# Kernel optimization log

Measured on AMD Instinct MI355X. Metric: run time of the kernel, lower is better.

The kernel has to match this reference:

```python
import jax, jax.numpy as jnp
import numpy as np

B, S, D = 16, 512, 768      # batch, max_n_words, context_dim (input_size)
E, R = 128, 2048            # entities per doc, candidate relations per doc
H = 768                     # config.hidden_size
H2 = H // 2                 # 384
OUT = 2                     # binary relation classes


def _linear_params(k, fan_in, fan_out):
    k1, k2 = jax.random.split(k)
    bound = 1.0 / np.sqrt(fan_in)
    W = jax.random.uniform(k1, (fan_in, fan_out), minval=-bound, maxval=bound, dtype=jnp.float32)
    b = jax.random.uniform(k2, (fan_out,), minval=-bound, maxval=bound, dtype=jnp.float32)
    return W, b


def setup_inputs() -> dict:
    key = jax.random.key(0)
    ks = jax.random.split(key, 16)
    hW1, hb1 = _linear_params(ks[0], 2 * D, H)
    hW2, hb2 = _linear_params(ks[1], H, H2)
    tW1, tb1 = _linear_params(ks[2], 2 * D, H)
    tW2, tb2 = _linear_params(ks[3], H, H2)
    bnd = 1.0 / np.sqrt(H2)
    bil_w = jax.random.uniform(ks[4], (OUT, H2, H2), minval=-bnd, maxval=bnd, dtype=jnp.float32)
    lW, lb = _linear_params(ks[5], 2 * H2, OUT)
    emb = jax.random.normal(ks[6], (3, D), dtype=jnp.float32)  # entity_emb
    hidden_states = jax.random.normal(ks[7], (B, S, D), dtype=jnp.float32)
    ent_start = jax.random.randint(ks[8], (B, E), 0, S)
    ent_label = jax.random.randint(ks[9], (B, E), 0, 3)
    rel_head = jax.random.randint(ks[10], (B, R), 0, E)
    rel_tail = jax.random.randint(ks[11], (B, R), 0, E)
    rel_label = jax.random.randint(ks[12], (B, R), 0, 2)
    return dict(hidden_states=hidden_states, emb=emb,
                hW1=hW1, hb1=hb1, hW2=hW2, hb2=hb2,
                tW1=tW1, tb1=tb1, tW2=tW2, tb2=tb2,
                bil_w=bil_w, lW=lW, lb=lb,
                ent_start=ent_start, ent_label=ent_label,
                rel_head=rel_head, rel_tail=rel_tail, rel_label=rel_label)


def reference(hidden_states, emb, hW1, hb1, hW2, hb2, tW1, tb1, tW2, tb2,
              bil_w, lW, lb, ent_start, ent_label, rel_head, rel_tail, rel_label):
    def tower(rel_idx, W1, b1, W2, b2):
        start = jnp.take_along_axis(ent_start, rel_idx, axis=1)              # [B,R]
        lab = jnp.take_along_axis(ent_label, rel_idx, axis=1)                # [B,R]
        hid = jnp.take_along_axis(hidden_states, start[..., None], axis=1)   # [B,R,D]
        rep = jnp.concatenate([hid, emb[lab]], axis=-1)                      # [B,R,2D]
        h = jax.nn.relu(rep @ W1 + b1)                                       # [B,R,H]
        return jax.nn.relu(h @ W2 + b2)                                      # [B,R,H2]

    heads = tower(rel_head, hW1, hb1, hW2, hb2)
    tails = tower(rel_tail, tW1, tb1, tW2, tb2)
    # Biaffine: bilinear (no bias) + linear over concat
    logits = (jnp.einsum('bri,oij,brj->bro', heads, bil_w, tails)
              + jnp.concatenate([heads, tails], axis=-1) @ lW + lb)          # [B,R,2]
    logp = jax.nn.log_softmax(logits, axis=-1)
    loss = -jnp.mean(jnp.take_along_axis(logp, rel_label[..., None], axis=-1))
    return loss, logits
```

## Files before the change

### kernel.cpp

```cpp
#include <hip/hip_runtime.h>
#include <hip/hip_bf16.h>
#include <cstdint>

typedef unsigned short ushort_t;
typedef __bf16 bf16x8 __attribute__((ext_vector_type(8)));
typedef float f32x4 __attribute__((ext_vector_type(4)));

#define B_   16
#define S_   512
#define D_   768
#define E_   128
#define R_   2048
#define NREL 32768

__device__ inline ushort_t f2b(float f) {
    uint32_t u = __builtin_bit_cast(uint32_t, f);
    uint32_t r = (u + 0x7fffu + ((u >> 16) & 1u)) >> 16;
    return (ushort_t)r;
}
__device__ inline float b2f(ushort_t u) {
    uint32_t v = ((uint32_t)u) << 16;
    return __builtin_bit_cast(float, v);
}
__device__ inline float bl(uint32_t u) {
    uint32_t v = u << 16;
    return __builtin_bit_cast(float, v);
}
__device__ inline float bh(uint32_t u) {
    uint32_t v = u & 0xffff0000u;
    return __builtin_bit_cast(float, v);
}

__global__ __launch_bounds__(256) void prep_kernel(
    const float* __restrict__ hidden, const float* __restrict__ emb,
    const float* __restrict__ lW,
    const int* __restrict__ ent_start, const int* __restrict__ ent_label,
    ushort_t* __restrict__ repE, ushort_t* __restrict__ BmatT,
    ushort_t* __restrict__ lWtT, float* __restrict__ out)
{
    int idx = blockIdx.x * 256 + threadIdx.x;
    if (idx == 0) out[0] = 0.0f;
    if (idx < 786432) {
        int row = idx / 384, q = idx - row * 384;
        int c = q * 4;
        int b = row >> 7;
        int st = ent_start[row], lab = ent_label[row];
        const float* srcp = (c < 768)
            ? hidden + ((size_t)(b * S_ + st) * D_ + c)
            : emb + ((size_t)lab * D_ + (c - 768));
        float4 v = *reinterpret_cast<const float4*>(srcp);
        uint32_t lo = (uint32_t)f2b(v.x) | ((uint32_t)f2b(v.y) << 16);
        uint32_t hi = (uint32_t)f2b(v.z) | ((uint32_t)f2b(v.w) << 16);
        uint2 pk; pk.x = lo; pk.y = hi;
        *reinterpret_cast<uint2*>(repE + (size_t)idx * 4) = pk;
        return;
    }
    int i2 = idx - 786432;
    if (i2 < 768) {
        int o = i2 / 384, kk = i2 - o * 384;
        BmatT[(768 + o) * 384 + kk] = f2b(lW[kk * 2 + o]);
        return;
    }
    i2 -= 768;
    if (i2 < 768) {
        int o = i2 / 384, ii = i2 - o * 384;
        lWtT[o * 384 + ii] = f2b(lW[(384 + ii) * 2 + o]);
    }
}

__global__ __launch_bounds__(256) void transpose_w(
    const float* __restrict__ hW1, const float* __restrict__ tW1,
    const float* __restrict__ hW2, const float* __restrict__ tW2,
    const float* __restrict__ bil,
    ushort_t* __restrict__ hW1T, ushort_t* __restrict__ tW1T,
    ushort_t* __restrict__ hW2T, ushort_t* __restrict__ tW2T,
    ushort_t* __restrict__ BmatT)
{
    __shared__ float tile[32][33];
    int z = blockIdx.z;
    const float* src; ushort_t* dst; int Rr, Cc;
    switch (z) {
        case 0:  src = hW1;          dst = hW1T;           Rr = 1536; Cc = 768; break;
        case 1:  src = tW1;          dst = tW1T;           Rr = 1536; Cc = 768; break;
        case 2:  src = hW2;          dst = hW2T;           Rr = 768;  Cc = 384; break;
        case 3:  src = tW2;          dst = tW2T;           Rr = 768;  Cc = 384; break;
        case 4:  src = bil;          dst = BmatT;          Rr = 384;  Cc = 384; break;
        default: src = bil + 147456; dst = BmatT + 147456; Rr = 384;  Cc = 384; break;
    }
    int tR = blockIdx.x * 32, tC = blockIdx.y * 32;
    if (tR >= Rr || tC >= Cc) return;
    int tx = threadIdx.x & 31, ty = threadIdx.x >> 5;
#pragma unroll
    for (int r = 0; r < 4; ++r)
        tile[ty + r * 8][tx] = src[(size_t)(tR + ty + r * 8) * Cc + tC + tx];
    __syncthreads();
#pragma unroll
    for (int r = 0; r < 4; ++r)
        dst[(size_t)(tC + ty + r * 8) * Rr + tR + tx] = f2b(tile[tx][ty + r * 8]);
}

__global__ __launch_bounds__(256) void gemm_lds(
    const ushort_t* __restrict__ A0, const ushort_t* __restrict__ A1,
    const ushort_t* __restrict__ Bt0, const ushort_t* __restrict__ Bt1,
    const float* __restrict__ bias0, const float* __restrict__ bias1,
    ushort_t* __restrict__ out0, ushort_t* __restrict__ out1,
    int M, int N, int K, int doRelu)
{
    __shared__ ushort_t As[64 * 32];
    __shared__ ushort_t Bs[64 * 32];
    const ushort_t* A   = blockIdx.z ? A1 : A0;
    const ushort_t* Bt  = blockIdx.z ? Bt1 : Bt0;
    const float*   bias = blockIdx.z ? bias1 : bias0;
    ushort_t*      out  = blockIdx.z ? out1 : out0;

    int t = threadIdx.x;
    int lane = t & 63, wave = t >> 6;
    int tileM = blockIdx.x * 64, tileN = blockIdx.y * 64;
    int wm = (wave >> 1) * 32, wn = (wave & 1) * 32;
    int l15 = lane & 15, quad = lane >> 4;

    const ushort_t* gA = A  + (size_t)tileM * K;
    const ushort_t* gB = Bt + (size_t)tileN * K;

    int srow = t >> 2, sc8 = (t & 3) << 3;

    f32x4 acc[2][2];
#pragma unroll
    for (int a = 0; a < 2; ++a)
#pragma unroll
        for (int b = 0; b < 2; ++b) {
            acc[a][b][0] = 0.f; acc[a][b][1] = 0.f;
            acc[a][b][2] = 0.f; acc[a][b][3] = 0.f;
        }

    for (int k0 = 0; k0 < K; k0 += 32) {
        __builtin_amdgcn_global_load_lds(
            (const __attribute__((address_space(1))) void*)(gA + (size_t)srow * K + k0 + sc8),
            (__attribute__((address_space(3))) void*)(As + t * 8), 16, 0, 0);
        __builtin_amdgcn_global_load_lds(
            (const __attribute__((address_space(1))) void*)(gB + (size_t)srow * K + k0 + sc8),
            (__attribute__((address_space(3))) void*)(Bs + t * 8), 16, 0, 0);
        __syncthreads();
        bf16x8 af[2], bfr[2];
#pragma unroll
        for (int mi = 0; mi < 2; ++mi)
            af[mi] = *reinterpret_cast<const bf16x8*>(As + (wm + mi * 16 + l15) * 32 + quad * 8);
#pragma unroll
        for (int ni = 0; ni < 2; ++ni)
            bfr[ni] = *reinterpret_cast<const bf16x8*>(Bs + (wn + ni * 16 + l15) * 32 + quad * 8);
#pragma unroll
        for (int mi = 0; mi < 2; ++mi)
#pragma unroll
            for (int ni = 0; ni < 2; ++ni)
                acc[mi][ni] = __builtin_amdgcn_mfma_f32_16x16x32_bf16(af[mi], bfr[ni], acc[mi][ni], 0, 0, 0);
        __syncthreads();
    }

#pragma unroll
    for (int mi = 0; mi < 2; ++mi) {
        int gr = tileM + wm + mi * 16 + quad * 4;
#pragma unroll
        for (int ni = 0; ni < 2; ++ni) {
            int gc = tileN + wn + ni * 16 + l15;
            if (gc < N) {
                float bb = bias ? bias[gc] : 0.0f;
#pragma unroll
                for (int r = 0; r < 4; ++r) {
                    float v = acc[mi][ni][r] + bb;
                    if (doRelu) v = fmaxf(v, 0.0f);
                    out[(size_t)(gr + r) * N + gc] = f2b(v);
                }
            }
        }
    }
}

__global__ __launch_bounds__(256) void rel_kernel(
    const ushort_t* __restrict__ Uext, const ushort_t* __restrict__ tailsE,
    const ushort_t* __restrict__ lWtT, const float* __restrict__ lb,
    const int* __restrict__ rel_head, const int* __restrict__ rel_tail,
    const int* __restrict__ rel_label, float* __restrict__ out)
{
    __shared__ float wsum[4];
    int lane = threadIdx.x & 63, wave = threadIdx.x >> 6;
    const uint32_t* lw32 = reinterpret_cast<const uint32_t*>(lWtT);
    float lb0 = lb[0], lb1 = lb[1];
    float lossAcc = 0.0f;
    int base = (blockIdx.x * 4 + wave) * 8;

    for (int q = 0; q < 8; ++q) {
        int rel = base + q;
        int b = rel >> 11;
        int h = rel_head[rel], t = rel_tail[rel], lab = rel_label[rel];
        const uint32_t* uh = reinterpret_cast<const uint32_t*>(Uext + (size_t)(b * E_ + h) * 770);
        const uint32_t* tv = reinterpret_cast<const uint32_t*>(tailsE + (size_t)(b * E_ + t) * 384);

        float a0 = 0.f, a1 = 0.f, w0s = 0.f, w1s = 0.f;
#pragma unroll
        for (int j = 0; j < 3; ++j) {
            int i = lane + 64 * j;
            uint32_t tu = tv[i];
            uint32_t u0 = uh[i], u1 = uh[192 + i];
            uint32_t q0 = lw32[i], q1 = lw32[192 + i];
            float tl = bl(tu), th = bh(tu);
            a0  += tl * bl(u0) + th * bh(u0);
            a1  += tl * bl(u1) + th * bh(u1);
            w0s += tl * bl(q0) + th * bh(q0);
            w1s += tl * bl(q1) + th * bh(q1);
        }
#pragma unroll
        for (int d = 1; d < 64; d <<= 1) {
            a0  += __shfl_xor(a0, d);
            a1  += __shfl_xor(a1, d);
            w0s += __shfl_xor(w0s, d);
            w1s += __shfl_xor(w1s, d);
        }
        const ushort_t* uhs = reinterpret_cast<const ushort_t*>(uh);
        float l0v = a0 + w0s + b2f(uhs[768]) + lb0;
        float l1v = a1 + w1s + b2f(uhs[769]) + lb1;
        if (lane == 0) {
            out[1 + 2 * rel]     = l0v;
            out[1 + 2 * rel + 1] = l1v;
        }
        float m = fmaxf(l0v, l1v);
        float lse = m + logf(expf(l0v - m) + expf(l1v - m));
        lossAcc += lse - (lab ? l1v : l0v);
    }
    if (lane == 0) wsum[wave] = lossAcc;
    __syncthreads();
    if (threadIdx.x == 0) {
        float s = wsum[0] + wsum[1] + wsum[2] + wsum[3];
        atomicAdd(out, s * (1.0f / 32768.0f));
    }
}

extern "C" void kernel_launch(void* const* d_in, const int* in_sizes, int n_in,
                              void* d_out, int out_size, void* d_ws, size_t ws_size,
                              hipStream_t stream)
{
    const float* hidden = (const float*)d_in[0];
    const float* emb    = (const float*)d_in[1];
    const float* hW1    = (const float*)d_in[2];
    const float* hb1    = (const float*)d_in[3];
    const float* hW2    = (const float*)d_in[4];
    const float* hb2    = (const float*)d_in[5];
    const float* tW1    = (const float*)d_in[6];
    const float* tb1    = (const float*)d_in[7];
    const float* tW2    = (const float*)d_in[8];
    const float* tb2    = (const float*)d_in[9];
    const float* bil    = (const float*)d_in[10];
    const float* lW     = (const float*)d_in[11];
    const float* lb     = (const float*)d_in[12];
    const int* ent_start = (const int*)d_in[13];
    const int* ent_label = (const int*)d_in[14];
    const int* rel_head  = (const int*)d_in[15];
    const int* rel_tail  = (const int*)d_in[16];
    const int* rel_label = (const int*)d_in[17];
    float* out = (float*)d_out;

    char* ws = (char*)d_ws;
    ushort_t* repE   = (ushort_t*)(ws + 0);
    ushort_t* hW1T   = (ushort_t*)(ws + 6291456);
    ushort_t* tW1T   = (ushort_t*)(ws + 8650752);
    ushort_t* hW2T   = (ushort_t*)(ws + 11010048);
    ushort_t* tW2T   = (ushort_t*)(ws + 11599872);
    ushort_t* BmatT  = (ushort_t*)(ws + 12189696);
    ushort_t* lWtT   = (ushort_t*)(ws + 12781056);
    ushort_t* h1     = (ushort_t*)(ws + 12782592);
    ushort_t* t1     = (ushort_t*)(ws + 15928320);
    ushort_t* headsE = (ushort_t*)(ws + 19074048);
    ushort_t* tailsE = (ushort_t*)(ws + 20646912);
    ushort_t* Uext   = (ushort_t*)(ws + 22219776);

    prep_kernel<<<3078, 256, 0, stream>>>(
        hidden, emb, lW, ent_start, ent_label, repE, BmatT, lWtT, out);

    transpose_w<<<dim3(48, 24, 6), 256, 0, stream>>>(
        hW1, tW1, hW2, tW2, bil, hW1T, tW1T, hW2T, tW2T, BmatT);

    gemm_lds<<<dim3(32, 12, 2), 256, 0, stream>>>(
        repE, repE, hW1T, tW1T, hb1, tb1, h1, t1, 2048, 768, 1536, 1);

    gemm_lds<<<dim3(32, 6, 2), 256, 0, stream>>>(
        h1, t1, hW2T, tW2T, hb2, tb2, headsE, tailsE, 2048, 384, 768, 1);

    gemm_lds<<<dim3(32, 13, 1), 256, 0, stream>>>(
        headsE, headsE, BmatT, BmatT, nullptr, nullptr, Uext, Uext, 2048, 770, 384, 0);

    rel_kernel<<<1024, 256, 0, stream>>>(
        Uext, tailsE, lWtT, lb, rel_head, rel_tail, rel_label, out);
}
```

Measured before the change: 181.0 us.

## Fold entity embedding into per-label bias and precompute tail linear term

Since the embedding half of the concatenated input takes only three distinct rows, its product with W1 is precomputed as three per-label bias vectors. The first GEMM's K dimension drops from 1536 to 768, and the gathered input buffer is half the size. The tail part of the final linear layer is also computed once per entity as an extra z-slice of the bilinear GEMM, rather than per relation inside rel_kernel. This adds a small serial dot-product path in the transpose kernel and an indexed bias load in the GEMM epilogue.

```diff
diff --git a/kernel.cpp b/kernel.cpp
--- a/kernel.cpp
+++ b/kernel.cpp
@@ -32,22 +32,19 @@
 }
 
 __global__ __launch_bounds__(256) void prep_kernel(
-    const float* __restrict__ hidden, const float* __restrict__ emb,
-    const float* __restrict__ lW,
-    const int* __restrict__ ent_start, const int* __restrict__ ent_label,
+    const float* __restrict__ hidden, const float* __restrict__ lW,
+    const int* __restrict__ ent_start,
     ushort_t* __restrict__ repE, ushort_t* __restrict__ BmatT,
     ushort_t* __restrict__ lWtT, float* __restrict__ out)
 {
     int idx = blockIdx.x * 256 + threadIdx.x;
     if (idx == 0) out[0] = 0.0f;
-    if (idx < 786432) {
-        int row = idx / 384, q = idx - row * 384;
+    if (idx < 393216) {
+        int row = idx / 192, q = idx - row * 192;
         int c = q * 4;
         int b = row >> 7;
-        int st = ent_start[row], lab = ent_label[row];
-        const float* srcp = (c < 768)
-            ? hidden + ((size_t)(b * S_ + st) * D_ + c)
-            : emb + ((size_t)lab * D_ + (c - 768));
+        int st = ent_start[row];
+        const float* srcp = hidden + ((size_t)(b * S_ + st) * D_ + c);
         float4 v = *reinterpret_cast<const float4*>(srcp);
         uint32_t lo = (uint32_t)f2b(v.x) | ((uint32_t)f2b(v.y) << 16);
         uint32_t hi = (uint32_t)f2b(v.z) | ((uint32_t)f2b(v.w) << 16);
@@ -55,7 +52,7 @@
         *reinterpret_cast<uint2*>(repE + (size_t)idx * 4) = pk;
         return;
     }
-    int i2 = idx - 786432;
+    int i2 = idx - 393216;
     if (i2 < 768) {
         int o = i2 / 384, kk = i2 - o * 384;
         BmatT[(768 + o) * 384 + kk] = f2b(lW[kk * 2 + o]);
@@ -71,51 +68,90 @@
 __global__ __launch_bounds__(256) void transpose_w(
     const float* __restrict__ hW1, const float* __restrict__ tW1,
     const float* __restrict__ hW2, const float* __restrict__ tW2,
-    const float* __restrict__ bil,
+    const float* __restrict__ bil, const float* __restrict__ emb,
+    const float* __restrict__ hb1, const float* __restrict__ tb1,
     ushort_t* __restrict__ hW1T, ushort_t* __restrict__ tW1T,
     ushort_t* __restrict__ hW2T, ushort_t* __restrict__ tW2T,
-    ushort_t* __restrict__ BmatT)
-{
-    __shared__ float tile[32][33];
+    ushort_t* __restrict__ BmatT,
+    float* __restrict__ biasEh, float* __restrict__ biasEt)
+{
+    __shared__ float smem[1056];
     int z = blockIdx.z;
+    if (z >= 6) {
+        if (blockIdx.y || blockIdx.x >= 12) return;
+        const float* W1 = (z == 6) ? hW1 : tW1;
+        const float* b1 = (z == 6) ? hb1 : tb1;
+        float* dstB     = (z == 6) ? biasEh : biasEt;
+        int c64 = threadIdx.x & 63, kc = threadIdx.x >> 6;
+        int col = blockIdx.x * 64 + c64;
+        float a0 = 0.f, a1 = 0.f, a2 = 0.f;
+        const float* wp = W1 + (size_t)(768 + kc * 192) * 768 + col;
+        const float* e0 = emb + kc * 192;
+        for (int k = 0; k < 192; ++k) {
+            float w = wp[(size_t)k * 768];
+            a0 += e0[k] * w;
+            a1 += e0[768 + k] * w;
+            a2 += e0[1536 + k] * w;
+        }
+        smem[(kc * 3 + 0) * 64 + c64] = a0;
+        smem[(kc * 3 + 1) * 64 + c64] = a1;
+        smem[(kc * 3 + 2) * 64 + c64] = a2;
+        __syncthreads();
+        if (kc == 0) {
+            float bv = b1[col];
+#pragma unroll
+            for (int l = 0; l < 3; ++l) {
+                float s = smem[l * 64 + c64] + smem[(3 + l) * 64 + c64]
+                        + smem[(6 + l) * 64 + c64] + smem[(9 + l) * 64 + c64];
+                dstB[l * 768 + col] = bv + s;
+            }
+        }
+        return;
+    }
     const float* src; ushort_t* dst; int Rr, Cc;
     switch (z) {
-        case 0:  src = hW1;          dst = hW1T;           Rr = 1536; Cc = 768; break;
-        case 1:  src = tW1;          dst = tW1T;           Rr = 1536; Cc = 768; break;
-        case 2:  src = hW2;          dst = hW2T;           Rr = 768;  Cc = 384; break;
-        case 3:  src = tW2;          dst = tW2T;           Rr = 768;  Cc = 384; break;
-        case 4:  src = bil;          dst = BmatT;          Rr = 384;  Cc = 384; break;
-        default: src = bil + 147456; dst = BmatT + 147456; Rr = 384;  Cc = 384; break;
+        case 0:  src = hW1;          dst = hW1T;           Rr = 768; Cc = 768; break;
+        case 1:  src = tW1;          dst = tW1T;           Rr = 768; Cc = 768; break;
+        case 2:  src = hW2;          dst = hW2T;           Rr = 768; Cc = 384; break;
+        case 3:  src = tW2;          dst = tW2T;           Rr = 768; Cc = 384; break;
+        case 4:  src = bil;          dst = BmatT;          Rr = 384; Cc = 384; break;
+        default: src = bil + 147456; dst = BmatT + 147456; Rr = 384; Cc = 384; break;
     }
     int tR = blockIdx.x * 32, tC = blockIdx.y * 32;
     if (tR >= Rr || tC >= Cc) return;
     int tx = threadIdx.x & 31, ty = threadIdx.x >> 5;
 #pragma unroll
     for (int r = 0; r < 4; ++r)
-        tile[ty + r * 8][tx] = src[(size_t)(tR + ty + r * 8) * Cc + tC + tx];
+        smem[(ty + r * 8) * 33 + tx] = src[(size_t)(tR + ty + r * 8) * Cc + tC + tx];
     __syncthreads();
 #pragma unroll
     for (int r = 0; r < 4; ++r)
-        dst[(size_t)(tC + ty + r * 8) * Rr + tR + tx] = f2b(tile[tx][ty + r * 8]);
+        dst[(size_t)(tC + ty + r * 8) * Rr + tR + tx] = f2b(smem[tx * 33 + ty + r * 8]);
 }
 
 __global__ __launch_bounds__(256) void gemm_lds(
     const ushort_t* __restrict__ A0, const ushort_t* __restrict__ A1,
     const ushort_t* __restrict__ Bt0, const ushort_t* __restrict__ Bt1,
     const float* __restrict__ bias0, const float* __restrict__ bias1,
-    ushort_t* __restrict__ out0, ushort_t* __restrict__ out1,
-    int M, int N, int K, int doRelu)
+    void* __restrict__ out0, void* __restrict__ out1,
+    const int* __restrict__ lab,
+    int M, int N0, int N1, int K, int doRelu, int f32o0, int f32o1)
 {
     __shared__ ushort_t As[64 * 32];
     __shared__ ushort_t Bs[64 * 32];
+    int N = blockIdx.z ? N1 : N0;
+    int tileN = blockIdx.y * 64;
+    if (tileN >= N) return;
     const ushort_t* A   = blockIdx.z ? A1 : A0;
     const ushort_t* Bt  = blockIdx.z ? Bt1 : Bt0;
     const float*   bias = blockIdx.z ? bias1 : bias0;
-    ushort_t*      out  = blockIdx.z ? out1 : out0;
+    int           f32o  = blockIdx.z ? f32o1 : f32o0;
+    ushort_t*      outH = (ushort_t*)(blockIdx.z ? out1 : out0);
+    float*         outF = (float*)(blockIdx.z ? out1 : out0);
 
     int t = threadIdx.x;
     int lane = t & 63, wave = t >> 6;
-    int tileM = blockIdx.x * 64, tileN = blockIdx.y * 64;
+    int tileM = blockIdx.x * 64;
     int wm = (wave >> 1) * 32, wn = (wave & 1) * 32;
     int l15 = lane & 15, quad = lane >> 4;
 
@@ -159,16 +195,23 @@
 #pragma unroll
     for (int mi = 0; mi < 2; ++mi) {
         int gr = tileM + wm + mi * 16 + quad * 4;
+        int lb4[4];
+        if (lab) {
+#pragma unroll
+            for (int r = 0; r < 4; ++r) lb4[r] = lab[gr + r];
+        }
 #pragma unroll
         for (int ni = 0; ni < 2; ++ni) {
             int gc = tileN + wn + ni * 16 + l15;
             if (gc < N) {
-                float bb = bias ? bias[gc] : 0.0f;
 #pragma unroll
                 for (int r = 0; r < 4; ++r) {
+                    float bb = lab ? bias[(size_t)lb4[r] * N + gc]
+                                   : (bias ? bias[gc] : 0.0f);
                     float v = acc[mi][ni][r] + bb;
                     if (doRelu) v = fmaxf(v, 0.0f);
-                    out[(size_t)(gr + r) * N + gc] = f2b(v);
+                    if (f32o) outF[(size_t)(gr + r) * N + gc] = v;
+                    else      outH[(size_t)(gr + r) * N + gc] = f2b(v);
                 }
             }
         }
@@ -177,13 +220,12 @@
 
 __global__ __launch_bounds__(256) void rel_kernel(
     const ushort_t* __restrict__ Uext, const ushort_t* __restrict__ tailsE,
-    const ushort_t* __restrict__ lWtT, const float* __restrict__ lb,
+    const float* __restrict__ tLin, const float* __restrict__ lb,
     const int* __restrict__ rel_head, const int* __restrict__ rel_tail,
     const int* __restrict__ rel_label, float* __restrict__ out)
 {
     __shared__ float wsum[4];
     int lane = threadIdx.x & 63, wave = threadIdx.x >> 6;
-    const uint32_t* lw32 = reinterpret_cast<const uint32_t*>(lWtT);
     float lb0 = lb[0], lb1 = lb[1];
     float lossAcc = 0.0f;
     int base = (blockIdx.x * 4 + wave) * 8;
@@ -195,29 +237,25 @@
         const uint32_t* uh = reinterpret_cast<const uint32_t*>(Uext + (size_t)(b * E_ + h) * 770);
         const uint32_t* tv = reinterpret_cast<const uint32_t*>(tailsE + (size_t)(b * E_ + t) * 384);
 
-        float a0 = 0.f, a1 = 0.f, w0s = 0.f, w1s = 0.f;
+        float a0 = 0.f, a1 = 0.f;
 #pragma unroll
         for (int j = 0; j < 3; ++j) {
             int i = lane + 64 * j;
             uint32_t tu = tv[i];
             uint32_t u0 = uh[i], u1 = uh[192 + i];
-            uint32_t q0 = lw32[i], q1 = lw32[192 + i];
             float tl = bl(tu), th = bh(tu);
-            a0  += tl * bl(u0) + th * bh(u0);
-            a1  += tl * bl(u1) + th * bh(u1);
-            w0s += tl * bl(q0) + th * bh(q0);
-            w1s += tl * bl(q1) + th * bh(q1);
+            a0 += tl * bl(u0) + th * bh(u0);
+            a1 += tl * bl(u1) + th * bh(u1);
         }
 #pragma unroll
         for (int d = 1; d < 64; d <<= 1) {
-            a0  += __shfl_xor(a0, d);
-            a1  += __shfl_xor(a1, d);
-            w0s += __shfl_xor(w0s, d);
-            w1s += __shfl_xor(w1s, d);
+            a0 += __shfl_xor(a0, d);
+            a1 += __shfl_xor(a1, d);
         }
         const ushort_t* uhs = reinterpret_cast<const ushort_t*>(uh);
-        float l0v = a0 + w0s + b2f(uhs[768]) + lb0;
-        float l1v = a1 + w1s + b2f(uhs[769]) + lb1;
+        float2 tp = reinterpret_cast<const float2*>(tLin)[b * E_ + t];
+        float l0v = a0 + tp.x + b2f(uhs[768]) + lb0;
+        float l1v = a1 + tp.y + b2f(uhs[769]) + lb1;
         if (lane == 0) {
             out[1 + 2 * rel]     = l0v;
             out[1 + 2 * rel + 1] = l1v;
@@ -260,33 +298,40 @@
 
     char* ws = (char*)d_ws;
     ushort_t* repE   = (ushort_t*)(ws + 0);
-    ushort_t* hW1T   = (ushort_t*)(ws + 6291456);
-    ushort_t* tW1T   = (ushort_t*)(ws + 8650752);
-    ushort_t* hW2T   = (ushort_t*)(ws + 11010048);
-    ushort_t* tW2T   = (ushort_t*)(ws + 11599872);
-    ushort_t* BmatT  = (ushort_t*)(ws + 12189696);
-    ushort_t* lWtT   = (ushort_t*)(ws + 12781056);
-    ushort_t* h1     = (ushort_t*)(ws + 12782592);
-    ushort_t* t1     = (ushort_t*)(ws + 15928320);
-    ushort_t* headsE = (ushort_t*)(ws + 19074048);
-    ushort_t* tailsE = (ushort_t*)(ws + 20646912);
-    ushort_t* Uext   = (ushort_t*)(ws + 22219776);
-
-    prep_kernel<<<3078, 256, 0, stream>>>(
-        hidden, emb, lW, ent_start, ent_label, repE, BmatT, lWtT, out);
-
-    transpose_w<<<dim3(48, 24, 6), 256, 0, stream>>>(
-        hW1, tW1, hW2, tW2, bil, hW1T, tW1T, hW2T, tW2T, BmatT);
+    ushort_t* hW1T   = (ushort_t*)(ws + 3145728);
+    ushort_t* tW1T   = (ushort_t*)(ws + 4325376);
+    ushort_t* hW2T   = (ushort_t*)(ws + 5505024);
+    ushort_t* tW2T   = (ushort_t*)(ws + 6094848);
+    ushort_t* BmatT  = (ushort_t*)(ws + 6684672);
+    ushort_t* lWtT   = (ushort_t*)(ws + 7276032);
+    float*    biasEh = (float*)   (ws + 7277568);
+    float*    biasEt = (float*)   (ws + 7286784);
+    float*    tLin   = (float*)   (ws + 7296000);
+    ushort_t* h1     = (ushort_t*)(ws + 7312384);
+    ushort_t* t1     = (ushort_t*)(ws + 10458112);
+    ushort_t* headsE = (ushort_t*)(ws + 13603840);
+    ushort_t* tailsE = (ushort_t*)(ws + 15176704);
+    ushort_t* Uext   = (ushort_t*)(ws + 16749568);
+
+    prep_kernel<<<1542, 256, 0, stream>>>(
+        hidden, lW, ent_start, repE, BmatT, lWtT, out);
+
+    transpose_w<<<dim3(24, 24, 8), 256, 0, stream>>>(
+        hW1, tW1, hW2, tW2, bil, emb, hb1, tb1,
+        hW1T, tW1T, hW2T, tW2T, BmatT, biasEh, biasEt);
 
     gemm_lds<<<dim3(32, 12, 2), 256, 0, stream>>>(
-        repE, repE, hW1T, tW1T, hb1, tb1, h1, t1, 2048, 768, 1536, 1);
+        repE, repE, hW1T, tW1T, biasEh, biasEt, h1, t1, ent_label,
+        2048, 768, 768, 768, 1, 0, 0);
 
     gemm_lds<<<dim3(32, 6, 2), 256, 0, stream>>>(
-        h1, t1, hW2T, tW2T, hb2, tb2, headsE, tailsE, 2048, 384, 768, 1);
-
-    gemm_lds<<<dim3(32, 13, 1), 256, 0, stream>>>(
-        headsE, headsE, BmatT, BmatT, nullptr, nullptr, Uext, Uext, 2048, 770, 384, 0);
+        h1, t1, hW2T, tW2T, hb2, tb2, headsE, tailsE, nullptr,
+        2048, 384, 384, 768, 1, 0, 0);
+
+    gemm_lds<<<dim3(32, 13, 2), 256, 0, stream>>>(
+        headsE, tailsE, BmatT, lWtT, nullptr, nullptr, Uext, tLin, nullptr,
+        2048, 770, 2, 384, 0, 0, 1);
 
     rel_kernel<<<1024, 256, 0, stream>>>(
-        Uext, tailsE, lWtT, lb, rel_head, rel_tail, rel_label, out);
-}
+        Uext, tailsE, tLin, lb, rel_head, rel_tail, rel_label, out);
+}
```

After: 188.7 us. 4.3% more time.
